# Optimization experiments

Measured on AMD Instinct MI355X. Metric: run time of the kernel, lower is better.

Reference implementation:

```python
import jax, jax.numpy as jnp
import numpy as np
import math

K_BRANCH = 8  # config['k']

def _selectors(n, k):
    # Static (trace-time) construction of per-level gather indices, mask=True branch.
    L = math.ceil(math.log(n) / math.log(k)) + 1
    rel = [0] + [math.ceil(n / k ** i) for i in range(L)]  # level sizes, leaves first
    Li = np.cumsum(np.array(rel))                          # level start offsets in node dim
    sels = []
    for l in range(L):
        m = rel[l + 1]
        i = np.arange(m)[:, None]
        anc = None
        if l < L - 1:
            m_next = rel[l + 2]
            j = np.arange(m_next)[None, :]
            cond = (j + 1) / m_next <= i / m
            anc = np.where(cond, Li[l + 1] + j, 0)
        s = np.arange(k)[None, :]
        ridx = np.minimum(i // k * k + s, m - 1)
        sib = np.where(ridx <= i, Li[l] + ridx, 0)  # rel/m <= i/m  <=>  rel <= i
        chi = None
        if l >= 1:
            m_prev = rel[l]
            c = np.arange(k)[None, :]
            ridx = np.minimum(i * k + c, m_prev - 1)
            cond = ridx / m_prev <= i / m
            chi = np.where(cond, Li[l - 1] + ridx, 0)
        sels.append((anc, sib, chi))
    return L, Li, sels

def _sdp(q, Kmat, Vmat, sel, d):
    keys = Kmat[:, :, sel, :]   # [b,h,m,w,d] gather
    vals = Vmat[:, :, sel, :]
    logits = jnp.einsum('bhnd,bhnkd->bhnk', q, keys) / math.sqrt(d)
    w = jax.nn.softmax(logits, axis=-1)
    return jnp.einsum('bhnk,bhnkd->bhnd', w, vals)

def setup_inputs() -> dict:
    key = jax.random.key(0)
    k1, k2, k3 = jax.random.split(key, 3)
    b, h, n_tot, d = 2, 4, 585, 128
    return {
        'Q': jax.random.normal(k1, (b, h, n_tot, d), dtype=jnp.float32),
        'K': jax.random.normal(k2, (b, h, n_tot, d), dtype=jnp.float32),
        'V': jax.random.normal(k3, (b, h, n_tot, d), dtype=jnp.float32),
        'n': 512,
    }

def reference(Q, K, V, n):
    k = K_BRANCH
    d = Q.shape[-1]
    L, Li, sels = _selectors(int(n), k)
    # Sequential bottom-up level updates: V at level l is rewritten before level l+1 reads it.
    for l in range(L):
        anc, sib, chi = sels[l]
        q = Q[:, :, Li[l]:Li[l + 1], :]
        out = _sdp(q, K, V, sib, d)
        if anc is not None:
            out = out + _sdp(q, K, V, anc, d)
        if chi is not None:
            out = out + _sdp(q, K, V, chi, d)
        V = V.at[:, :, Li[l]:Li[l + 1], :].set(out / 3.0)
    return V
```

## Files before the change

### kernel.cpp

```cpp
#include <hip/hip_runtime.h>
#include <math.h>

#define D 128
#define NTOT 585
#define SCALE 0.08838834764831845f
#define THIRD 0.33333333333333333f

__device__ __forceinline__ float rsum_c(float v) {
    v += __shfl_xor(v, 1, 64);
    v += __shfl_xor(v, 2, 64);
    v += __shfl_xor(v, 4, 64);
    return v;
}
__device__ __forceinline__ float rsum_s(float v) {
    v += __shfl_xor(v, 8, 64);
    v += __shfl_xor(v, 16, 64);
    v += __shfl_xor(v, 32, 64);
    return v;
}
__device__ __forceinline__ float rmax_s(float v) {
    v = fmaxf(v, __shfl_xor(v, 8, 64));
    v = fmaxf(v, __shfl_xor(v, 16, 64));
    v = fmaxf(v, __shfl_xor(v, 32, 64));
    return v;
}
__device__ __forceinline__ float dot16(const float4 q[4], const float* __restrict__ row, int c) {
    const float4* k = (const float4*)(row + (c << 4));
    float4 k0 = k[0], k1 = k[1], k2 = k[2], k3 = k[3];
    float p0 = q[0].x * k0.x + q[0].y * k0.y + q[0].z * k0.z + q[0].w * k0.w;
    float p1 = q[1].x * k1.x + q[1].y * k1.y + q[1].z * k1.z + q[1].w * k1.w;
    float p2 = q[2].x * k2.x + q[2].y * k2.y + q[2].z * k2.z + q[2].w * k2.w;
    float p3 = q[3].x * k3.x + q[3].y * k3.y + q[3].z * k3.z + q[3].w * k3.w;
    return (p0 + p1) + (p2 + p3);
}
__device__ __forceinline__ void vacc(float w, const float* __restrict__ row, int c, float4 acc[4]) {
    const float4* v = (const float4*)(row + (c << 4));
#pragma unroll
    for (int u = 0; u < 4; ++u) {
        float4 t = v[u];
        acc[u].x += w * t.x; acc[u].y += w * t.y; acc[u].z += w * t.z; acc[u].w += w * t.w;
    }
}
__device__ __forceinline__ void vacc_reg(float w, const float4 vv[4], float4 acc[4]) {
#pragma unroll
    for (int u = 0; u < 4; ++u) {
        acc[u].x += w * vv[u].x; acc[u].y += w * vv[u].y;
        acc[u].z += w * vv[u].z; acc[u].w += w * vv[u].w;
    }
}
__device__ __forceinline__ void loadq(const float* __restrict__ qrow, int c, float4 q[4]) {
    const float4* qp = (const float4*)(qrow + (c << 4));
#pragma unroll
    for (int u = 0; u < 4; ++u) q[u] = qp[u];
}
__device__ __forceinline__ void butterfly_acc(float4 acc[4]) {
#pragma unroll
    for (int u = 0; u < 4; ++u) {
        acc[u].x = rsum_s(acc[u].x);
        acc[u].y = rsum_s(acc[u].y);
        acc[u].z = rsum_s(acc[u].z);
        acc[u].w = rsum_s(acc[u].w);
    }
}

__device__ __forceinline__ void l0_slim(int i, int s, int c,
                                        const float* __restrict__ Qb,
                                        const float* __restrict__ Kb,
                                        const float* __restrict__ Vb,
                                        float4 acc[4]) {
    float4 q4[4];
    loadq(Qb + (size_t)i * D, c, q4);
#pragma unroll
    for (int u = 0; u < 4; ++u) acc[u] = make_float4(0.f, 0.f, 0.f, 0.f);
    const float lg0 = rsum_c(dot16(q4, Kb, c)) * SCALE;
    const int sl = i & 7;
    const int g = i >> 3;

    {
        float lg = -1e30f;
        if (s <= sl)
            lg = rsum_c(dot16(q4, Kb + (size_t)(8 * g + s) * D, c)) * SCALE;
        const float m = fmaxf(rmax_s(lg), lg0);
        const float e = (s <= sl) ? __expf(lg - m) : 0.f;
        const float e0 = __expf(lg0 - m);
        float zp = e;
        if (s == 0) zp += (float)(7 - sl) * e0;
        const float inv = 1.f / rsum_s(zp);
        if (s <= sl) vacc(e * inv, Vb + (size_t)(8 * g + s) * D, c, acc);
        if (s == 0 && sl < 7) vacc((float)(7 - sl) * e0 * inv, Vb, c, acc);
    }

    {
        float lgA[8];
        float mloc = lg0;
#pragma unroll
        for (int R = 0; R < 4; ++R) {
            if (16 * R < g) {
#pragma unroll
                for (int rr = 0; rr < 2; ++rr) {
                    const int r = 2 * R + rr;
                    const int j = 8 * r + s;
                    float lg = -1e30f;
                    if (j < g)
                        lg = rsum_c(dot16(q4, Kb + (size_t)(512 + j) * D, c)) * SCALE;
                    lgA[r] = lg;
                    mloc = fmaxf(mloc, lg);
                }
            } else { lgA[2 * R] = -1e30f; lgA[2 * R + 1] = -1e30f; }
        }
        const float m = rmax_s(mloc);
        const float e0 = __expf(lg0 - m);
        float zp = (s == 0) ? (float)(64 - g) * e0 : 0.f;
        float eA[8];
#pragma unroll
        for (int R = 0; R < 4; ++R) {
            if (16 * R < g) {
#pragma unroll
                for (int rr = 0; rr < 2; ++rr) {
                    const int r = 2 * R + rr;
                    eA[r] = (lgA[r] > -1e29f) ? __expf(lgA[r] - m) : 0.f;
                    zp += eA[r];
                }
            }
        }
        const float inv = 1.f / rsum_s(zp);
#pragma unroll
        for (int R = 0; R < 4; ++R) {
            if (16 * R < g) {
#pragma unroll
                for (int rr = 0; rr < 2; ++rr) {
                    const int r = 2 * R + rr;
                    const int j = 8 * r + s;
                    if (j < g) vacc(eA[r] * inv, Vb + (size_t)(512 + j) * D, c, acc);
                }
            }
        }
        if (s == 0) vacc((float)(64 - g) * e0 * inv, Vb, c, acc);
    }
    butterfly_acc(acc);
}

__global__ __launch_bounds__(256) void sequoia_onepass(const float* __restrict__ Q,
                                                       const float* __restrict__ K,
                                                       const float* __restrict__ V,
                                                       float* __restrict__ Out) {
    const int gwave = (blockIdx.x * 256 + threadIdx.x) >> 6;
    const int lane = threadIdx.x & 63;
    const int s = lane >> 3, c = lane & 7;

    if (gwave >= 512) {
        const int w = gwave - 512;
        const int i = w & 511;
        const int bh = w >> 9;
        const float* Qb = Q + (size_t)bh * NTOT * D;
        const float* Kb = K + (size_t)bh * NTOT * D;
        const float* Vb = V + (size_t)bh * NTOT * D;
        float* Ob = Out + (size_t)bh * NTOT * D;
        float4 acc[4];
        l0_slim(i, s, c, Qb, Kb, Vb, acc);
        if (s == 0) {
            float4* orow = (float4*)(Ob + (size_t)i * D + (c << 4));
#pragma unroll
            for (int u = 0; u < 4; ++u)
                orow[u] = make_float4(acc[u].x * THIRD, acc[u].y * THIRD,
                                      acc[u].z * THIRD, acc[u].w * THIRD);
        }
        return;
    }

    const int t = gwave;
    const int i = t & 63;
    const int bh = t >> 6;
    const float* Qb = Q + (size_t)bh * NTOT * D;
    const float* Kb = K + (size_t)bh * NTOT * D;
    const float* Vb = V + (size_t)bh * NTOT * D;
    float* Ob = Out + (size_t)bh * NTOT * D;

    float4 v0n[4];
    {
        const float4* vp = (const float4*)(Vb + (c << 4));
#pragma unroll
        for (int u = 0; u < 4; ++u) {
            float4 v = vp[u];
            v0n[u] = make_float4(v.x * (2.f * THIRD), v.y * (2.f * THIRD),
                                 v.z * (2.f * THIRD), v.w * (2.f * THIRD));
        }
    }

    float4 o0[4];
    if (i == 0) {
#pragma unroll
        for (int u = 0; u < 4; ++u) o0[u] = v0n[u];
    } else {
        float4 tmp[4];
        l0_slim(8 * i, s, c, Qb, Kb, Vb, tmp);
#pragma unroll
        for (int u = 0; u < 4; ++u)
            o0[u] = make_float4(tmp[u].x * THIRD, tmp[u].y * THIRD,
                                tmp[u].z * THIRD, tmp[u].w * THIRD);
    }

    float4 o1[4];
    {
        float4 q1[4];
        loadq(Qb + (size_t)(512 + i) * D, c, q1);
        float4 acc[4] = {{0,0,0,0},{0,0,0,0},{0,0,0,0},{0,0,0,0}};
        const float lg0q = rsum_c(dot16(q1, Kb, c)) * SCALE;
        const int sl1 = i & 7;
        const int gq = i >> 3;
        {
            const int r = (i & ~7) + s;
            float lg = -1e30f;
            if (s <= sl1)
                lg = rsum_c(dot16(q1, Kb + (size_t)(512 + r) * D, c)) * SCALE;
            const float m = fmaxf(rmax_s(lg), lg0q);
            const float e = (s <= sl1) ? __expf(lg - m) : 0.f;
            const float e0 = __expf(lg0q - m);
            float zp = e;
            if (s == 0) zp += (float)(7 - sl1) * e0;
            const float inv = 1.f / rsum_s(zp);
            if (s <= sl1) vacc(e * inv, Vb + (size_t)(512 + r) * D, c, acc);
            if (s == 0 && sl1 < 7) vacc_reg((float)(7 - sl1) * e0 * inv, v0n, acc);
        }
        {
            float lg = -1e30f;
            if (s < gq)
                lg = rsum_c(dot16(q1, Kb + (size_t)(576 + s) * D, c)) * SCALE;
            const float m = fmaxf(rmax_s(lg), lg0q);
            const float e = (s < gq) ? __expf(lg - m) : 0.f;
            const float e0 = __expf(lg0q - m);
            float zp = e;
            if (s == 0) zp += (float)(8 - gq) * e0;
            const float inv = 1.f / rsum_s(zp);
            if (s < gq) vacc(e * inv, Vb + (size_t)(576 + s) * D, c, acc);
            if (s == 0) vacc_reg((float)(8 - gq) * e0 * inv, v0n, acc);
        }
        {
            float lg = -1e30f;
            if (s == 0)
                lg = rsum_c(dot16(q1, Kb + (size_t)(8 * i) * D, c)) * SCALE;
            const float m = fmaxf(rmax_s(lg), lg0q);
            const float e = (s == 0) ? __expf(lg - m) : 0.f;
            const float e0 = __expf(lg0q - m);
            const float zp = (s == 0) ? (e + 7.f * e0) : 0.f;
            const float inv = 1.f / rsum_s(zp);
            if (s == 0) {
                vacc_reg(e * inv, o0, acc);
                vacc_reg(7.f * e0 * inv, v0n, acc);
            }
        }
        butterfly_acc(acc);
#pragma unroll
        for (int u = 0; u < 4; ++u)
            o1[u] = make_float4(acc[u].x * THIRD, acc[u].y * THIRD,
                                acc[u].z * THIRD, acc[u].w * THIRD);
        if (s == 0) {
            float4* orow = (float4*)(Ob + (size_t)(512 + i) * D + (c << 4));
#pragma unroll
            for (int u = 0; u < 4; ++u) orow[u] = o1[u];
        }
    }

    if ((i & 7) == 0) {
        const int j = i >> 3;
        float4 q2[4];
        loadq(Qb + (size_t)(576 + j) * D, c, q2);
        float4 acc[4] = {{0,0,0,0},{0,0,0,0},{0,0,0,0},{0,0,0,0}};
        const float lg0q = rsum_c(dot16(q2, Kb, c)) * SCALE;
        {
            float lg = -1e30f;
            if (s <= j)
                lg = rsum_c(dot16(q2, Kb + (size_t)(576 + s) * D, c)) * SCALE;
            const float m = fmaxf(rmax_s(lg), lg0q);
            const float e = (s <= j) ? __expf(lg - m) : 0.f;
            const float e0 = __expf(lg0q - m);
            float zp = e;
            if (s == 0) zp += (float)(7 - j) * e0;
            const float inv = 1.f / rsum_s(zp);
            if (s <= j) vacc(e * inv, Vb + (size_t)(576 + s) * D, c, acc);
            if (s == 0 && j < 7) vacc_reg((float)(7 - j) * e0 * inv, v0n, acc);
        }
        {
            float lg = -1e30f;
            if (s == 0)
                lg = rsum_c(dot16(q2, Kb + (size_t)(512 + 8 * j) * D, c)) * SCALE;
            const float m = fmaxf(rmax_s(lg), lg0q);
            const float e = (s == 0) ? __expf(lg - m) : 0.f;
            const float e0 = __expf(lg0q - m);
            const float zp = (s == 0) ? (e + 7.f * e0) : 0.f;
            const float inv = 1.f / rsum_s(zp);
            if (s == 0) {
                vacc_reg(e * inv, o1, acc);
                vacc_reg(7.f * e0 * inv, v0n, acc);
            }
        }
        butterfly_acc(acc);
        float4 o2[4];
#pragma unroll
        for (int u = 0; u < 4; ++u)
            o2[u] = make_float4((acc[u].x + v0n[u].x) * THIRD, (acc[u].y + v0n[u].y) * THIRD,
                                (acc[u].z + v0n[u].z) * THIRD, (acc[u].w + v0n[u].w) * THIRD);
        if (s == 0) {
            float4* orow = (float4*)(Ob + (size_t)(576 + j) * D + (c << 4));
#pragma unroll
            for (int u = 0; u < 4; ++u) orow[u] = o2[u];
        }

        if (j == 0) {
            float4 q3[4];
            loadq(Qb + (size_t)584 * D, c, q3);
            const float lg0q = rsum_c(dot16(q3, Kb, c)) * SCALE;
            float lg = -1e30f;
            if (s == 0)
                lg = rsum_c(dot16(q3, Kb + (size_t)576 * D, c)) * SCALE;
            const float m = fmaxf(rmax_s(lg), lg0q);
            const float e = (s == 0) ? __expf(lg - m) : 0.f;
            const float e0 = __expf(lg0q - m);
            const float zp = (s == 0) ? (e + 7.f * e0) : 0.f;
            const float inv = 1.f / rsum_s(zp);
            float4 acc3[4] = {{0,0,0,0},{0,0,0,0},{0,0,0,0},{0,0,0,0}};
            if (s == 0) {
                vacc_reg(e * inv, o2, acc3);
                vacc_reg(7.f * e0 * inv, v0n, acc3);
            }
            butterfly_acc(acc3);
            if (s == 0) {
                const float4* v584 = (const float4*)(Vb + (size_t)584 * D + (c << 4));
                float4* orow = (float4*)(Ob + (size_t)584 * D + (c << 4));
#pragma unroll
                for (int u = 0; u < 4; ++u) {
                    float4 bb = v584[u];
                    orow[u] = make_float4((acc3[u].x + bb.x) * THIRD,
                                          (acc3[u].y + bb.y) * THIRD,
                                          (acc3[u].z + bb.z) * THIRD,
                                          (acc3[u].w + bb.w) * THIRD);
                }
            }
        }
    }
}

extern "C" void kernel_launch(void* const* d_in, const int* in_sizes, int n_in,
                              void* d_out, int out_size, void* d_ws, size_t ws_size,
                              hipStream_t stream) {
    const float* Q = (const float*)d_in[0];
    const float* K = (const float*)d_in[1];
    const float* V = (const float*)d_in[2];
    float* Out = (float*)d_out;
    hipLaunchKernelGGL(sequoia_onepass, dim3(1152), dim3(256), 0, stream, Q, K, V, Out);
}
```

Measured before the change: 85.29 us.

## Split level-0 into LDS-staged kernel and reuse its output for upper levels

Level-0 attention moves into its own kernel. Each 1024-thread block stages 16 sibling rows, the 64 level-1 ancestor rows and the padding row of K and V into shared memory, then serves 16 queries from that tile. The upper-level kernel no longer recomputes level-0 outputs for its child nodes; it reads them back from the output buffer written by the first kernel. This removes redundant work and repeated global/L2 reads, but adds a second launch and a hard dependency between the two kernels.

```diff
diff --git a/kernel.cpp b/kernel.cpp
--- a/kernel.cpp
+++ b/kernel.cpp
@@ -5,6 +5,7 @@
 #define NTOT 585
 #define SCALE 0.08838834764831845f
 #define THIRD 0.33333333333333333f
+#define LROW 132
 
 __device__ __forceinline__ float rsum_c(float v) {
     v += __shfl_xor(v, 1, 64);
@@ -63,31 +64,53 @@
     }
 }
 
-__device__ __forceinline__ void l0_slim(int i, int s, int c,
-                                        const float* __restrict__ Qb,
-                                        const float* __restrict__ Kb,
-                                        const float* __restrict__ Vb,
-                                        float4 acc[4]) {
+__global__ __launch_bounds__(1024) void level0_lds(const float* __restrict__ Q,
+                                                   const float* __restrict__ K,
+                                                   const float* __restrict__ V,
+                                                   float* __restrict__ Out) {
+    __shared__ float Ks[81 * LROW];
+    __shared__ float Vs[81 * LROW];
+    const int tid = threadIdx.x;
+    const int lane = tid & 63;
+    const int s = lane >> 3, c = lane & 7;
+    const int bh = blockIdx.x >> 5;
+    const int qb0 = (blockIdx.x & 31) << 4;
+    const float* Qb = Q + (size_t)bh * NTOT * D;
+    const float* Kb = K + (size_t)bh * NTOT * D;
+    const float* Vb = V + (size_t)bh * NTOT * D;
+    float* Ob = Out + (size_t)bh * NTOT * D;
+
+    for (int t = tid; t < 81 * 32; t += 1024) {
+        const int row = t >> 5, col = (t & 31) << 2;
+        const int src = (row < 16) ? (qb0 + row) : ((row < 80) ? (512 + row - 16) : 0);
+        *(float4*)(&Ks[row * LROW + col]) = *(const float4*)(Kb + (size_t)src * D + col);
+        *(float4*)(&Vs[row * LROW + col]) = *(const float4*)(Vb + (size_t)src * D + col);
+    }
+    __syncthreads();
+
+    const int w = tid >> 6;
+    const int i = qb0 + w;
+    const int sl = i & 7;
+    const int g = i >> 3;
+    const int sibbase = w & 8;
+
     float4 q4[4];
     loadq(Qb + (size_t)i * D, c, q4);
-#pragma unroll
-    for (int u = 0; u < 4; ++u) acc[u] = make_float4(0.f, 0.f, 0.f, 0.f);
-    const float lg0 = rsum_c(dot16(q4, Kb, c)) * SCALE;
-    const int sl = i & 7;
-    const int g = i >> 3;
+    float4 acc[4] = {{0,0,0,0},{0,0,0,0},{0,0,0,0},{0,0,0,0}};
+    const float lg0 = rsum_c(dot16(q4, &Ks[80 * LROW], c)) * SCALE;
 
     {
         float lg = -1e30f;
         if (s <= sl)
-            lg = rsum_c(dot16(q4, Kb + (size_t)(8 * g + s) * D, c)) * SCALE;
+            lg = rsum_c(dot16(q4, &Ks[(sibbase + s) * LROW], c)) * SCALE;
         const float m = fmaxf(rmax_s(lg), lg0);
         const float e = (s <= sl) ? __expf(lg - m) : 0.f;
         const float e0 = __expf(lg0 - m);
         float zp = e;
         if (s == 0) zp += (float)(7 - sl) * e0;
         const float inv = 1.f / rsum_s(zp);
-        if (s <= sl) vacc(e * inv, Vb + (size_t)(8 * g + s) * D, c, acc);
-        if (s == 0 && sl < 7) vacc((float)(7 - sl) * e0 * inv, Vb, c, acc);
+        if (s <= sl) vacc(e * inv, &Vs[(sibbase + s) * LROW], c, acc);
+        if (s == 0 && sl < 7) vacc((float)(7 - sl) * e0 * inv, &Vs[80 * LROW], c, acc);
     }
 
     {
@@ -102,7 +125,7 @@
                     const int j = 8 * r + s;
                     float lg = -1e30f;
                     if (j < g)
-                        lg = rsum_c(dot16(q4, Kb + (size_t)(512 + j) * D, c)) * SCALE;
+                        lg = rsum_c(dot16(q4, &Ks[(16 + j) * LROW], c)) * SCALE;
                     lgA[r] = lg;
                     mloc = fmaxf(mloc, lg);
                 }
@@ -131,73 +154,42 @@
                 for (int rr = 0; rr < 2; ++rr) {
                     const int r = 2 * R + rr;
                     const int j = 8 * r + s;
-                    if (j < g) vacc(eA[r] * inv, Vb + (size_t)(512 + j) * D, c, acc);
+                    if (j < g) vacc(eA[r] * inv, &Vs[(16 + j) * LROW], c, acc);
                 }
             }
         }
-        if (s == 0) vacc((float)(64 - g) * e0 * inv, Vb, c, acc);
+        if (s == 0) vacc((float)(64 - g) * e0 * inv, &Vs[80 * LROW], c, acc);
     }
     butterfly_acc(acc);
-}
-
-__global__ __launch_bounds__(256) void sequoia_onepass(const float* __restrict__ Q,
+    if (s == 0) {
+        float4* orow = (float4*)(Ob + (size_t)i * D + (c << 4));
+#pragma unroll
+        for (int u = 0; u < 4; ++u)
+            orow[u] = make_float4(acc[u].x * THIRD, acc[u].y * THIRD,
+                                  acc[u].z * THIRD, acc[u].w * THIRD);
+    }
+}
+
+__global__ __launch_bounds__(256) void level123_kernel(const float* __restrict__ Q,
                                                        const float* __restrict__ K,
                                                        const float* __restrict__ V,
                                                        float* __restrict__ Out) {
     const int gwave = (blockIdx.x * 256 + threadIdx.x) >> 6;
     const int lane = threadIdx.x & 63;
     const int s = lane >> 3, c = lane & 7;
-
-    if (gwave >= 512) {
-        const int w = gwave - 512;
-        const int i = w & 511;
-        const int bh = w >> 9;
-        const float* Qb = Q + (size_t)bh * NTOT * D;
-        const float* Kb = K + (size_t)bh * NTOT * D;
-        const float* Vb = V + (size_t)bh * NTOT * D;
-        float* Ob = Out + (size_t)bh * NTOT * D;
-        float4 acc[4];
-        l0_slim(i, s, c, Qb, Kb, Vb, acc);
-        if (s == 0) {
-            float4* orow = (float4*)(Ob + (size_t)i * D + (c << 4));
-#pragma unroll
-            for (int u = 0; u < 4; ++u)
-                orow[u] = make_float4(acc[u].x * THIRD, acc[u].y * THIRD,
-                                      acc[u].z * THIRD, acc[u].w * THIRD);
-        }
-        return;
-    }
-
-    const int t = gwave;
-    const int i = t & 63;
-    const int bh = t >> 6;
+    const int i = gwave & 63;
+    const int bh = gwave >> 6;
     const float* Qb = Q + (size_t)bh * NTOT * D;
     const float* Kb = K + (size_t)bh * NTOT * D;
     const float* Vb = V + (size_t)bh * NTOT * D;
     float* Ob = Out + (size_t)bh * NTOT * D;
 
-    float4 v0n[4];
+    float4 v0n[4], o0[4];
     {
-        const float4* vp = (const float4*)(Vb + (c << 4));
-#pragma unroll
-        for (int u = 0; u < 4; ++u) {
-            float4 v = vp[u];
-            v0n[u] = make_float4(v.x * (2.f * THIRD), v.y * (2.f * THIRD),
-                                 v.z * (2.f * THIRD), v.w * (2.f * THIRD));
-        }
-    }
-
-    float4 o0[4];
-    if (i == 0) {
-#pragma unroll
-        for (int u = 0; u < 4; ++u) o0[u] = v0n[u];
-    } else {
-        float4 tmp[4];
-        l0_slim(8 * i, s, c, Qb, Kb, Vb, tmp);
-#pragma unroll
-        for (int u = 0; u < 4; ++u)
-            o0[u] = make_float4(tmp[u].x * THIRD, tmp[u].y * THIRD,
-                                tmp[u].z * THIRD, tmp[u].w * THIRD);
+        const float4* vp = (const float4*)(Ob + (c << 4));
+        const float4* op = (const float4*)(Ob + (size_t)(8 * i) * D + (c << 4));
+#pragma unroll
+        for (int u = 0; u < 4; ++u) { v0n[u] = vp[u]; o0[u] = op[u]; }
     }
 
     float4 o1[4];
@@ -309,13 +301,13 @@
         if (j == 0) {
             float4 q3[4];
             loadq(Qb + (size_t)584 * D, c, q3);
-            const float lg0q = rsum_c(dot16(q3, Kb, c)) * SCALE;
+            const float lg0r = rsum_c(dot16(q3, Kb, c)) * SCALE;
             float lg = -1e30f;
             if (s == 0)
                 lg = rsum_c(dot16(q3, Kb + (size_t)576 * D, c)) * SCALE;
-            const float m = fmaxf(rmax_s(lg), lg0q);
+            const float m = fmaxf(rmax_s(lg), lg0r);
             const float e = (s == 0) ? __expf(lg - m) : 0.f;
-            const float e0 = __expf(lg0q - m);
+            const float e0 = __expf(lg0r - m);
             const float zp = (s == 0) ? (e + 7.f * e0) : 0.f;
             const float inv = 1.f / rsum_s(zp);
             float4 acc3[4] = {{0,0,0,0},{0,0,0,0},{0,0,0,0},{0,0,0,0}};
@@ -347,5 +339,6 @@
     const float* K = (const float*)d_in[1];
     const float* V = (const float*)d_in[2];
     float* Out = (float*)d_out;
-    hipLaunchKernelGGL(sequoia_onepass, dim3(1152), dim3(256), 0, stream, Q, K, V, Out);
-}
+    hipLaunchKernelGGL(level0_lds, dim3(256), dim3(1024), 0, stream, Q, K, V, Out);
+    hipLaunchKernelGGL(level123_kernel, dim3(128), dim3(256), 0, stream, Q, K, V, Out);
+}
```

Result: faster. 79.50 us (-6.8%).
